# Optimization experiments

Hardware: AMD Instinct MI355X
Metric: run time of the kernel (lower is better)

Reference implementation:

```python
import jax, jax.numpy as jnp
import numpy as np

B, S, D = 2, 2048, 1024
H, HD = 16, 64          # num_heads, head_dim = D // H
C = 8                   # subspace_dim of the equivariant relative-position basis
EPS = 1e-6              # flax LayerNorm default epsilon


def setup_inputs() -> dict:
    key = jax.random.key(0)
    ks = jax.random.split(key, 12)
    sd = 0.02
    return {
        "x": jax.random.normal(ks[0], (B, S, D), jnp.float32),
        "Q_basis": jax.random.normal(ks[1], (S, S, C), jnp.float32),
        "Wq": jax.random.normal(ks[2], (D, H, HD), jnp.float32) * sd,
        "bq": jnp.zeros((H, HD), jnp.float32),
        "Wk": jax.random.normal(ks[3], (D, H, HD), jnp.float32) * sd,
        "bk": jnp.zeros((H, HD), jnp.float32),
        "Wv": jax.random.normal(ks[4], (D, H, HD), jnp.float32) * sd,
        "bv": jnp.zeros((H, HD), jnp.float32),
        "q_ln_scale": jnp.ones((HD,), jnp.float32),
        "k_ln_scale": jnp.ones((HD,), jnp.float32),
        "relative_attn": jax.random.normal(ks[5], (C, H), jnp.float32) * sd,
        "Wo": jax.random.normal(ks[6], (H, HD, D), jnp.float32) * sd,
        "bo": jnp.zeros((D,), jnp.float32),
    }


def _layernorm(x, scale):
    # LayerNorm over last axis, use_bias=False
    mu = jnp.mean(x, axis=-1, keepdims=True)
    var = jnp.mean(jnp.square(x - mu), axis=-1, keepdims=True)
    return (x - mu) * jax.lax.rsqrt(var + EPS) * scale


def reference(x, Q_basis, Wq, bq, Wk, bk, Wv, bv,
              q_ln_scale, k_ln_scale, relative_attn, Wo, bo):
    # QKV projections: [B,S,D] x [D,H,HD] -> [B,S,H,HD]
    q = jnp.einsum('bsd,dhk->bshk', x, Wq) + bq
    k = jnp.einsum('bsd,dhk->bshk', x, Wk) + bk
    v = jnp.einsum('bsd,dhk->bshk', x, Wv) + bv
    # QK layernorm over head_dim
    q = _layernorm(q, q_ln_scale)
    k = _layernorm(k, k_ln_scale)
    # Learned relative-position bias: [C,H] x [S,S,C] -> [H,S,S]
    bias = jnp.einsum('ch,qkc->hqk', relative_attn, Q_basis)
    # Scaled dot-product attention with bias (matches nn.dot_product_attention)
    scores = jnp.einsum('bqhd,bkhd->bhqk', q, k) / jnp.sqrt(jnp.float32(HD))
    attn = jax.nn.softmax(scores + bias, axis=-1)
    ctx = jnp.einsum('bhqk,bkhd->bqhd', attn, v)
    # Output projection over (heads, head_dim) -> D
    return jnp.einsum('bqhd,hdo->bqo', ctx, Wo) + bo
```

## Files before the change

kernel.cpp:

```cpp
#include <hip/hip_runtime.h>

typedef float f32x4 __attribute__((ext_vector_type(4)));
typedef __bf16 bf16x8 __attribute__((ext_vector_type(8)));
typedef unsigned short u16x8 __attribute__((ext_vector_type(8)));
typedef unsigned short u16x4 __attribute__((ext_vector_type(4)));

#define AS1 __attribute__((address_space(1)))
#define AS3 __attribute__((address_space(3)))

static __device__ __forceinline__ void gll16(const void* g, void* l) {
  __builtin_amdgcn_global_load_lds((const AS1 void*)g, (AS3 void*)l, 16, 0, 0);
}

static __device__ __forceinline__ float bf2f(unsigned short u) {
  unsigned int x = ((unsigned int)u) << 16;
  float f; __builtin_memcpy(&f, &x, 4); return f;
}
static __device__ __forceinline__ unsigned short f2bf(float f) {
  unsigned int x; __builtin_memcpy(&x, &f, 4);
  unsigned int r = (x + 0x7fffu + ((x >> 16) & 1u)) >> 16;
  return (unsigned short)r;
}

#define LOG2E 1.4426950408889634f
#define QSCALE (0.125f * LOG2E)

__global__ __launch_bounds__(256) void k_cvt_x(const float* __restrict__ x,
                                               unsigned short* __restrict__ xb) {
  int i = (blockIdx.x * 256 + threadIdx.x) * 4;
  float4 v = *(const float4*)(x + i);
  u16x4 o; o.x = f2bf(v.x); o.y = f2bf(v.y); o.z = f2bf(v.z); o.w = f2bf(v.w);
  *(u16x4*)(xb + i) = o;
}

__global__ __launch_bounds__(256) void k_transpose(const float* __restrict__ w0,
                                                   const float* __restrict__ w1,
                                                   const float* __restrict__ w2,
                                                   const float* __restrict__ w3,
                                                   unsigned short* __restrict__ dqkv,
                                                   unsigned short* __restrict__ dwo) {
  __shared__ float tile[32][33];
  int z = blockIdx.z;
  const float* src = (z == 0) ? w0 : (z == 1) ? w1 : (z == 2) ? w2 : w3;
  unsigned short* dst = (z < 3) ? (dqkv + (size_t)z * 1024 * 1024) : dwo;
  int tx = threadIdx.x, ty = threadIdx.y;
  int x0 = blockIdx.x * 32, y0 = blockIdx.y * 32;
#pragma unroll
  for (int i = 0; i < 4; ++i)
    tile[ty + 8 * i][tx] = src[(size_t)(y0 + ty + 8 * i) * 1024 + x0 + tx];
  __syncthreads();
#pragma unroll
  for (int i = 0; i < 4; ++i)
    dst[(size_t)(x0 + ty + 8 * i) * 1024 + y0 + tx] = f2bf(tile[tx][ty + 8 * i]);
}

__global__ __launch_bounds__(256) void k_bias(const float* __restrict__ Qb,
                                              const float* __restrict__ R,
                                              unsigned short* __restrict__ bias) {
  __shared__ float Rs[8][16];
  int t = threadIdx.x;
  if (t < 128) Rs[t >> 4][t & 15] = R[t] * LOG2E;
  __syncthreads();
  int q = blockIdx.x;
  int k = t * 8;
  const float* src = Qb + ((size_t)q * 2048 + k) * 8;
  float a[8][8];
#pragma unroll
  for (int kk = 0; kk < 8; ++kk) {
    float4 lo = *(const float4*)(src + kk * 8);
    float4 hi = *(const float4*)(src + kk * 8 + 4);
    a[kk][0] = lo.x; a[kk][1] = lo.y; a[kk][2] = lo.z; a[kk][3] = lo.w;
    a[kk][4] = hi.x; a[kk][5] = hi.y; a[kk][6] = hi.z; a[kk][7] = hi.w;
  }
#pragma unroll
  for (int h = 0; h < 16; ++h) {
    u16x8 o;
#pragma unroll
    for (int kk = 0; kk < 8; ++kk) {
      float s = 0.f;
#pragma unroll
      for (int c = 0; c < 8; ++c) s += a[kk][c] * Rs[c][h];
      o[kk] = f2bf(s);
    }
    *(u16x8*)(bias + ((size_t)h * 2048 + q) * 2048 + k) = o;
  }
}

__global__ __launch_bounds__(256) void k_qkv(const unsigned short* __restrict__ xb,
                                             const unsigned short* __restrict__ wt,
                                             const float* __restrict__ bq,
                                             const float* __restrict__ bk,
                                             const float* __restrict__ bv,
                                             const float* __restrict__ qls,
                                             const float* __restrict__ kls,
                                             unsigned short* __restrict__ qo,
                                             unsigned short* __restrict__ kqo,
                                             unsigned short* __restrict__ vo) {
  __shared__ unsigned short As[4096];
  __shared__ unsigned short Bs[4096];
  const int tid = threadIdx.x;
  const int w = tid >> 6, lane = tid & 63, quad = lane >> 4, lx = lane & 15;
  const int m0 = blockIdx.y * 128, n0 = blockIdx.x * 128;
  const int wrow = w >> 1, wcol = w & 1;

  f32x4 acc[4][4];
#pragma unroll
  for (int i = 0; i < 4; ++i)
#pragma unroll
    for (int j = 0; j < 4; ++j) acc[i][j] = (f32x4){0.f, 0.f, 0.f, 0.f};

  const unsigned short* ga = xb + (size_t)(m0 + 32 * w + (lane >> 2)) * 1024 + (lane & 3) * 8;
  const unsigned short* gb = wt + (size_t)(n0 + 32 * w + (lane >> 2)) * 1024 + (lane & 3) * 8;
  unsigned short* la = As + w * 1024;
  unsigned short* lb = Bs + w * 1024;

  for (int kt = 0; kt < 32; ++kt) {
    const int kofs = kt * 32;
    gll16(ga + kofs, la);
    gll16(ga + kofs + 16 * 1024, la + 512);
    gll16(gb + kofs, lb);
    gll16(gb + kofs + 16 * 1024, lb + 512);
    __syncthreads();
    bf16x8 af[4], bfr[4];
#pragma unroll
    for (int i = 0; i < 4; ++i)
      af[i] = *(const bf16x8*)&As[(64 * wrow + 16 * i + lx) * 32 + quad * 8];
#pragma unroll
    for (int j = 0; j < 4; ++j)
      bfr[j] = *(const bf16x8*)&Bs[(64 * wcol + 16 * j + lx) * 32 + quad * 8];
#pragma unroll
    for (int i = 0; i < 4; ++i)
#pragma unroll
      for (int j = 0; j < 4; ++j)
        acc[i][j] = __builtin_amdgcn_mfma_f32_16x16x32_bf16(af[i], bfr[j], acc[i][j], 0, 0, 0);
    __syncthreads();
  }

  const int colbase = n0 + 64 * wcol;
  const int region = colbase >> 10;
  const int h = (colbase & 1023) >> 6;
  const float* pbp = (region == 0) ? bq : (region == 1) ? bk : bv;
  float pb[4];
#pragma unroll
  for (int j = 0; j < 4; ++j) pb[j] = pbp[h * 64 + j * 16 + lx];

  if (region == 2) {
#pragma unroll
    for (int i = 0; i < 4; ++i) {
#pragma unroll
      for (int rr = 0; rr < 4; ++rr) {
        int m = m0 + 64 * wrow + 16 * i + quad * 4 + rr;
        int b = m >> 11, s = m & 2047;
        unsigned short* dst = vo + ((size_t)b * 16 + h) * 64 * 2048 + s;
#pragma unroll
        for (int j = 0; j < 4; ++j)
          dst[(size_t)(j * 16 + lx) * 2048] = f2bf(acc[i][j][rr] + pb[j]);
      }
    }
  } else {
    const float fac = region ? 1.0f : QSCALE;
    float scl[4];
    const float* lsp = region ? kls : qls;
#pragma unroll
    for (int j = 0; j < 4; ++j) scl[j] = lsp[j * 16 + lx] * fac;
    unsigned short* base = region ? kqo : qo;
#pragma unroll
    for (int i = 0; i < 4; ++i) {
#pragma unroll
      for (int rr = 0; rr < 4; ++rr) {
        int m = m0 + 64 * wrow + 16 * i + quad * 4 + rr;
        int b = m >> 11, s = m & 2047;
        float v0 = acc[i][0][rr] + pb[0];
        float v1 = acc[i][1][rr] + pb[1];
        float v2 = acc[i][2][rr] + pb[2];
        float v3 = acc[i][3][rr] + pb[3];
        float s1 = v0 + v1 + v2 + v3;
        float s2 = v0 * v0 + v1 * v1 + v2 * v2 + v3 * v3;
#pragma unroll
        for (int d = 1; d < 16; d <<= 1) {
          s1 += __shfl_xor(s1, d, 64);
          s2 += __shfl_xor(s2, d, 64);
        }
        float mu = s1 * 0.015625f;
        float var = s2 * 0.015625f - mu * mu;
        float ri = __builtin_amdgcn_rsqf(var + 1e-6f);
        unsigned short* dst = base + (((size_t)b * 16 + h) * 2048 + s) * 64;
        dst[0 * 16 + lx] = f2bf((v0 - mu) * ri * scl[0]);
        dst[1 * 16 + lx] = f2bf((v1 - mu) * ri * scl[1]);
        dst[2 * 16 + lx] = f2bf((v2 - mu) * ri * scl[2]);
        dst[3 * 16 + lx] = f2bf((v3 - mu) * ri * scl[3]);
      }
    }
  }
}

__global__ __launch_bounds__(256) void k_attn(const unsigned short* __restrict__ qp,
                                              const unsigned short* __restrict__ kp,
                                              const unsigned short* __restrict__ vp,
                                              const unsigned short* __restrict__ bp,
                                              unsigned short* __restrict__ ctx) {
  __shared__ unsigned short Qs[4096];
  __shared__ unsigned short Ks[4096];
  __shared__ unsigned short Vs[4096];
  __shared__ unsigned short Ps[4608];
  const int tid = threadIdx.x;
  const int w = tid >> 6, lane = tid & 63, quad = lane >> 4, lx = lane & 15;
  const int lx7 = lane & 7;
  const int qt = blockIdx.x, h = blockIdx.y, b = blockIdx.z;
  const int q0 = qt * 64;
  const size_t bh = (size_t)b * 16 + h;

  const unsigned short* qg = qp + (bh * 2048 + q0) * 64;
  gll16(qg + w * 512 + lane * 8, Qs + w * 512);
  gll16(qg + 2048 + w * 512 + lane * 8, Qs + 2048 + w * 512);
  __syncthreads();
  bf16x8 qf[2];
#pragma unroll
  for (int hh = 0; hh < 2; ++hh)
    qf[hh] = *(const bf16x8*)&Qs[(16 * w + lx) * 64 + hh * 32 + quad * 8];

  const unsigned short* kg = kp + bh * 2048 * 64;
  const unsigned short* vg = vp + bh * 64 * 2048;
  const unsigned short* bg = bp + ((size_t)h * 2048 + q0 + 16 * w + quad * 4) * 2048 + lx;

  const int rA = 16 * w + (lane >> 3);
  const int cA = (lane & 7) ^ (rA & 7);
  const unsigned short* kgA = kg + (size_t)rA * 64 + cA * 8;
  const unsigned short* kgB = kg + (size_t)(rA + 8) * 64 + cA * 8;
  const unsigned short* vgA = vg + (size_t)rA * 2048 + cA * 8;
  const unsigned short* vgB = vg + (size_t)(rA + 8) * 2048 + cA * 8;
  unsigned short* ldKA = Ks + w * 1024;
  unsigned short* ldKB = Ks + w * 1024 + 512;
  unsigned short* ldVA = Vs + w * 1024;
  unsigned short* ldVB = Vs + w * 1024 + 512;

  float l_run[4] = {0.f, 0.f, 0.f, 0.f};
  f32x4 acco[4];
#pragma unroll
  for (int j = 0; j < 4; ++j) acco[j] = (f32x4){0.f, 0.f, 0.f, 0.f};

  for (int kt = 0; kt < 32; ++kt) {
    const int k0 = kt * 64;
    gll16(kgA + (size_t)k0 * 64, ldKA);
    gll16(kgB + (size_t)k0 * 64, ldKB);
    gll16(vgA + k0, ldVA);
    gll16(vgB + k0, ldVB);
    unsigned short bu[4][4];
#pragma unroll
    for (int rr = 0; rr < 4; ++rr)
#pragma unroll
      for (int j = 0; j < 4; ++j) bu[rr][j] = bg[(size_t)rr * 2048 + k0 + j * 16];
    __syncthreads();

    f32x4 accs[4];
#pragma unroll
    for (int j = 0; j < 4; ++j)
#pragma unroll
      for (int rr = 0; rr < 4; ++rr) accs[j][rr] = bf2f(bu[rr][j]);
#pragma unroll
    for (int j = 0; j < 4; ++j) {
#pragma unroll
      for (int hh = 0; hh < 2; ++hh) {
        bf16x8 kf = *(const bf16x8*)&Ks[(j * 16 + lx) * 64 + ((hh * 4 + quad) ^ lx7) * 8];
        accs[j] = __builtin_amdgcn_mfma_f32_16x16x32_bf16(qf[hh], kf, accs[j], 0, 0, 0);
      }
    }
#pragma unroll
    for (int rr = 0; rr < 4; ++rr) {
      float p0 = __builtin_amdgcn_exp2f(accs[0][rr]);
      float p1 = __builtin_amdgcn_exp2f(accs[1][rr]);
      float p2 = __builtin_amdgcn_exp2f(accs[2][rr]);
      float p3 = __builtin_amdgcn_exp2f(accs[3][rr]);
      l_run[rr] += (p0 + p1) + (p2 + p3);
      unsigned short* pw = Ps + w * 1152 + (quad * 4 + rr) * 72 + lx;
      pw[0]  = f2bf(p0);
      pw[16] = f2bf(p1);
      pw[32] = f2bf(p2);
      pw[48] = f2bf(p3);
    }
    __asm__ volatile("s_waitcnt lgkmcnt(0)" ::: "memory");
    bf16x8 pf[2];
#pragma unroll
    for (int kh = 0; kh < 2; ++kh)
      pf[kh] = *(const bf16x8*)&Ps[w * 1152 + lx * 72 + kh * 32 + quad * 8];
#pragma unroll
    for (int j = 0; j < 4; ++j) {
#pragma unroll
      for (int kh = 0; kh < 2; ++kh) {
        bf16x8 vf = *(const bf16x8*)&Vs[(j * 16 + lx) * 64 + ((kh * 4 + quad) ^ lx7) * 8];
        acco[j] = __builtin_amdgcn_mfma_f32_16x16x32_bf16(pf[kh], vf, acco[j], 0, 0, 0);
      }
    }
    __syncthreads();
  }

#pragma unroll
  for (int rr = 0; rr < 4; ++rr) {
    float l = l_run[rr];
#pragma unroll
    for (int d = 1; d < 16; d <<= 1) l += __shfl_xor(l, d, 64);
    float rl = __builtin_amdgcn_rcpf(l);
    int s = q0 + 16 * w + quad * 4 + rr;
    unsigned short* dst = ctx + (((size_t)b * 2048 + s) * 16 + h) * 64;
#pragma unroll
    for (int j = 0; j < 4; ++j) dst[j * 16 + lx] = f2bf(acco[j][rr] * rl);
  }
}

__global__ __launch_bounds__(256) void k_out(const unsigned short* __restrict__ cx,
                                             const unsigned short* __restrict__ wt,
                                             const float* __restrict__ bo,
                                             float* __restrict__ out) {
  __shared__ unsigned short As[4096];
  __shared__ unsigned short Bs[4096];
  const int tid = threadIdx.x;
  const int w = tid >> 6, lane = tid & 63, quad = lane >> 4, lx = lane & 15;
  const int m0 = blockIdx.y * 128, n0 = blockIdx.x * 128;
  const int wrow = w >> 1, wcol = w & 1;

  f32x4 acc[4][4];
#pragma unroll
  for (int i = 0; i < 4; ++i)
#pragma unroll
    for (int j = 0; j < 4; ++j) acc[i][j] = (f32x4){0.f, 0.f, 0.f, 0.f};

  const unsigned short* ga = cx + (size_t)(m0 + 32 * w + (lane >> 2)) * 1024 + (lane & 3) * 8;
  const unsigned short* gb = wt + (size_t)(n0 + 32 * w + (lane >> 2)) * 1024 + (lane & 3) * 8;
  unsigned short* la = As + w * 1024;
  unsigned short* lb = Bs + w * 1024;

  for (int kt = 0; kt < 32; ++kt) {
    const int kofs = kt * 32;
    gll16(ga + kofs, la);
    gll16(ga + kofs + 16 * 1024, la + 512);
    gll16(gb + kofs, lb);
    gll16(gb + kofs + 16 * 1024, lb + 512);
    __syncthreads();
    bf16x8 af[4], bfr[4];
#pragma unroll
    for (int i = 0; i < 4; ++i)
      af[i] = *(const bf16x8*)&As[(64 * wrow + 16 * i + lx) * 32 + quad * 8];
#pragma unroll
    for (int j = 0; j < 4; ++j)
      bfr[j] = *(const bf16x8*)&Bs[(64 * wcol + 16 * j + lx) * 32 + quad * 8];
#pragma unroll
    for (int i = 0; i < 4; ++i)
#pragma unroll
      for (int j = 0; j < 4; ++j)
        acc[i][j] = __builtin_amdgcn_mfma_f32_16x16x32_bf16(af[i], bfr[j], acc[i][j], 0, 0, 0);
    __syncthreads();
  }

  const int colbase = n0 + 64 * wcol;
  float bb[4];
#pragma unroll
  for (int j = 0; j < 4; ++j) bb[j] = bo[colbase + j * 16 + lx];
#pragma unroll
  for (int i = 0; i < 4; ++i) {
#pragma unroll
    for (int rr = 0; rr < 4; ++rr) {
      int m = m0 + 64 * wrow + 16 * i + quad * 4 + rr;
      float* dst = out + (size_t)m * 1024 + colbase;
#pragma unroll
      for (int j = 0; j < 4; ++j) dst[j * 16 + lx] = acc[i][j][rr] + bb[j];
    }
  }
}

extern "C" void kernel_launch(void* const* d_in, const int* in_sizes, int n_in,
                              void* d_out, int out_size, void* d_ws, size_t ws_size,
                              hipStream_t stream) {
  (void)in_sizes; (void)n_in; (void)out_size; (void)ws_size;
  const float* x   = (const float*)d_in[0];
  const float* Qb  = (const float*)d_in[1];
  const float* Wq  = (const float*)d_in[2];
  const float* bq  = (const float*)d_in[3];
  const float* Wk  = (const float*)d_in[4];
  const float* bk  = (const float*)d_in[5];
  const float* Wv  = (const float*)d_in[6];
  const float* bv  = (const float*)d_in[7];
  const float* qls = (const float*)d_in[8];
  const float* kls = (const float*)d_in[9];
  const float* Ra  = (const float*)d_in[10];
  const float* Wo  = (const float*)d_in[11];
  const float* bo  = (const float*)d_in[12];
  float* out = (float*)d_out;

  char* ws = (char*)d_ws;
  unsigned short* xb    = (unsigned short*)(ws + 0);
  unsigned short* wqkvt = (unsigned short*)(ws + 8388608);
  unsigned short* wot   = (unsigned short*)(ws + 14680064);
  unsigned short* qb    = (unsigned short*)(ws + 16777216);
  unsigned short* kb    = (unsigned short*)(ws + 25165824);
  unsigned short* vtb   = (unsigned short*)(ws + 33554432);
  unsigned short* ctxb  = (unsigned short*)(ws + 41943040);
  unsigned short* biasb = (unsigned short*)(ws + 50331648);

  k_cvt_x<<<4096, 256, 0, stream>>>(x, xb);
  k_transpose<<<dim3(32, 32, 4), dim3(32, 8), 0, stream>>>(Wq, Wk, Wv, Wo, wqkvt, wot);
  k_bias<<<2048, 256, 0, stream>>>(Qb, Ra, biasb);
  k_qkv<<<dim3(24, 32), 256, 0, stream>>>(xb, wqkvt, bq, bk, bv, qls, kls, qb, kb, vtb);
  k_attn<<<dim3(32, 16, 2), 256, 0, stream>>>(qb, kb, vtb, biasb, ctxb);
  k_out<<<dim3(8, 32), 256, 0, stream>>>(ctxb, wot, bo, out);
}
```

Baseline: 454.4 us.

## Double-buffer LDS tiles in QKV, attention and output kernels with prefetch

Converts the GEMM and attention K/V loops to double-buffered LDS, issuing the global-to-LDS loads for the next tile before computing on the current one. The bias values for the next tile are also prefetched into registers. Q and P now share one LDS buffer, which keeps the extra LDS within budget, and P gets an XOR swizzle instead of padding. s_setprio is raised around the MFMA blocks. The aim is to hide global memory latency, at the cost of more LDS and registers, which may lower occupancy.

After: 436.0 us. 1.04x faster.

```diff
diff --git a/kernel.cpp b/kernel.cpp
--- a/kernel.cpp
+++ b/kernel.cpp
@@ -96,8 +96,8 @@
                                              unsigned short* __restrict__ qo,
                                              unsigned short* __restrict__ kqo,
                                              unsigned short* __restrict__ vo) {
-  __shared__ unsigned short As[4096];
-  __shared__ unsigned short Bs[4096];
+  __shared__ __align__(16) unsigned short As[8192];
+  __shared__ __align__(16) unsigned short Bs[8192];
   const int tid = threadIdx.x;
   const int w = tid >> 6, lane = tid & 63, quad = lane >> 4, lx = lane & 15;
   const int m0 = blockIdx.y * 128, n0 = blockIdx.x * 128;
@@ -111,28 +111,40 @@
 
   const unsigned short* ga = xb + (size_t)(m0 + 32 * w + (lane >> 2)) * 1024 + (lane & 3) * 8;
   const unsigned short* gb = wt + (size_t)(n0 + 32 * w + (lane >> 2)) * 1024 + (lane & 3) * 8;
-  unsigned short* la = As + w * 1024;
-  unsigned short* lb = Bs + w * 1024;
+
+  gll16(ga, As + w * 1024);
+  gll16(ga + 16 * 1024, As + w * 1024 + 512);
+  gll16(gb, Bs + w * 1024);
+  gll16(gb + 16 * 1024, Bs + w * 1024 + 512);
+  __syncthreads();
 
   for (int kt = 0; kt < 32; ++kt) {
-    const int kofs = kt * 32;
-    gll16(ga + kofs, la);
-    gll16(ga + kofs + 16 * 1024, la + 512);
-    gll16(gb + kofs, lb);
-    gll16(gb + kofs + 16 * 1024, lb + 512);
-    __syncthreads();
+    const int cur = kt & 1;
+    if (kt < 31) {
+      const int kofs = (kt + 1) * 32;
+      unsigned short* lan = As + (cur ^ 1) * 4096 + w * 1024;
+      unsigned short* lbn = Bs + (cur ^ 1) * 4096 + w * 1024;
+      gll16(ga + kofs, lan);
+      gll16(ga + kofs + 16 * 1024, lan + 512);
+      gll16(gb + kofs, lbn);
+      gll16(gb + kofs + 16 * 1024, lbn + 512);
+    }
+    const unsigned short* ac = As + cur * 4096;
+    const unsigned short* bc = Bs + cur * 4096;
     bf16x8 af[4], bfr[4];
 #pragma unroll
     for (int i = 0; i < 4; ++i)
-      af[i] = *(const bf16x8*)&As[(64 * wrow + 16 * i + lx) * 32 + quad * 8];
+      af[i] = *(const bf16x8*)&ac[(64 * wrow + 16 * i + lx) * 32 + quad * 8];
 #pragma unroll
     for (int j = 0; j < 4; ++j)
-      bfr[j] = *(const bf16x8*)&Bs[(64 * wcol + 16 * j + lx) * 32 + quad * 8];
+      bfr[j] = *(const bf16x8*)&bc[(64 * wcol + 16 * j + lx) * 32 + quad * 8];
+    __builtin_amdgcn_s_setprio(1);
 #pragma unroll
     for (int i = 0; i < 4; ++i)
 #pragma unroll
       for (int j = 0; j < 4; ++j)
         acc[i][j] = __builtin_amdgcn_mfma_f32_16x16x32_bf16(af[i], bfr[j], acc[i][j], 0, 0, 0);
+    __builtin_amdgcn_s_setprio(0);
     __syncthreads();
   }
 
@@ -199,10 +211,9 @@
                                               const unsigned short* __restrict__ vp,
                                               const unsigned short* __restrict__ bp,
                                               unsigned short* __restrict__ ctx) {
-  __shared__ unsigned short Qs[4096];
-  __shared__ unsigned short Ks[4096];
-  __shared__ unsigned short Vs[4096];
-  __shared__ unsigned short Ps[4608];
+  __shared__ __align__(16) unsigned short QPs[4096];
+  __shared__ __align__(16) unsigned short Ks[8192];
+  __shared__ __align__(16) unsigned short Vs[8192];
   const int tid = threadIdx.x;
   const int w = tid >> 6, lane = tid & 63, quad = lane >> 4, lx = lane & 15;
   const int lx7 = lane & 7;
@@ -211,13 +222,8 @@
   const size_t bh = (size_t)b * 16 + h;
 
   const unsigned short* qg = qp + (bh * 2048 + q0) * 64;
-  gll16(qg + w * 512 + lane * 8, Qs + w * 512);
-  gll16(qg + 2048 + w * 512 + lane * 8, Qs + 2048 + w * 512);
-  __syncthreads();
-  bf16x8 qf[2];
-#pragma unroll
-  for (int hh = 0; hh < 2; ++hh)
-    qf[hh] = *(const bf16x8*)&Qs[(16 * w + lx) * 64 + hh * 32 + quad * 8];
+  gll16(qg + w * 512 + lane * 8, QPs + w * 512);
+  gll16(qg + 2048 + w * 512 + lane * 8, QPs + 2048 + w * 512);
 
   const unsigned short* kg = kp + bh * 2048 * 64;
   const unsigned short* vg = vp + bh * 64 * 2048;
@@ -229,10 +235,23 @@
   const unsigned short* kgB = kg + (size_t)(rA + 8) * 64 + cA * 8;
   const unsigned short* vgA = vg + (size_t)rA * 2048 + cA * 8;
   const unsigned short* vgB = vg + (size_t)(rA + 8) * 2048 + cA * 8;
-  unsigned short* ldKA = Ks + w * 1024;
-  unsigned short* ldKB = Ks + w * 1024 + 512;
-  unsigned short* ldVA = Vs + w * 1024;
-  unsigned short* ldVB = Vs + w * 1024 + 512;
+
+  gll16(kgA, Ks + w * 1024);
+  gll16(kgB, Ks + w * 1024 + 512);
+  gll16(vgA, Vs + w * 1024);
+  gll16(vgB, Vs + w * 1024 + 512);
+  unsigned short bu[4][4], bun[4][4];
+#pragma unroll
+  for (int rr = 0; rr < 4; ++rr)
+#pragma unroll
+    for (int j = 0; j < 4; ++j) bu[rr][j] = bg[(size_t)rr * 2048 + j * 16];
+
+  __syncthreads();
+
+  bf16x8 qf[2];
+#pragma unroll
+  for (int hh = 0; hh < 2; ++hh)
+    qf[hh] = *(const bf16x8*)&QPs[(16 * w + lx) * 64 + hh * 32 + quad * 8];
 
   float l_run[4] = {0.f, 0.f, 0.f, 0.f};
   f32x4 acco[4];
@@ -240,31 +259,39 @@
   for (int j = 0; j < 4; ++j) acco[j] = (f32x4){0.f, 0.f, 0.f, 0.f};
 
   for (int kt = 0; kt < 32; ++kt) {
-    const int k0 = kt * 64;
-    gll16(kgA + (size_t)k0 * 64, ldKA);
-    gll16(kgB + (size_t)k0 * 64, ldKB);
-    gll16(vgA + k0, ldVA);
-    gll16(vgB + k0, ldVB);
-    unsigned short bu[4][4];
-#pragma unroll
-    for (int rr = 0; rr < 4; ++rr)
-#pragma unroll
-      for (int j = 0; j < 4; ++j) bu[rr][j] = bg[(size_t)rr * 2048 + k0 + j * 16];
-    __syncthreads();
+    const int cur = kt & 1;
+    const unsigned short* kc = Ks + cur * 4096;
+    const unsigned short* vc = Vs + cur * 4096;
+    if (kt < 31) {
+      const size_t k1 = (size_t)(kt + 1) * 64;
+      unsigned short* kn = Ks + (cur ^ 1) * 4096 + w * 1024;
+      unsigned short* vn = Vs + (cur ^ 1) * 4096 + w * 1024;
+      gll16(kgA + k1 * 64, kn);
+      gll16(kgB + k1 * 64, kn + 512);
+      gll16(vgA + k1, vn);
+      gll16(vgB + k1, vn + 512);
+#pragma unroll
+      for (int rr = 0; rr < 4; ++rr)
+#pragma unroll
+        for (int j = 0; j < 4; ++j) bun[rr][j] = bg[(size_t)rr * 2048 + k1 + j * 16];
+    }
 
     f32x4 accs[4];
 #pragma unroll
     for (int j = 0; j < 4; ++j)
 #pragma unroll
       for (int rr = 0; rr < 4; ++rr) accs[j][rr] = bf2f(bu[rr][j]);
+    __builtin_amdgcn_s_setprio(1);
 #pragma unroll
     for (int j = 0; j < 4; ++j) {
 #pragma unroll
       for (int hh = 0; hh < 2; ++hh) {
-        bf16x8 kf = *(const bf16x8*)&Ks[(j * 16 + lx) * 64 + ((hh * 4 + quad) ^ lx7) * 8];
+        bf16x8 kf = *(const bf16x8*)&kc[(j * 16 + lx) * 64 + ((hh * 4 + quad) ^ lx7) * 8];
         accs[j] = __builtin_amdgcn_mfma_f32_16x16x32_bf16(qf[hh], kf, accs[j], 0, 0, 0);
       }
     }
+    __builtin_amdgcn_s_setprio(0);
+
 #pragma unroll
     for (int rr = 0; rr < 4; ++rr) {
       float p0 = __builtin_amdgcn_exp2f(accs[0][rr]);
@@ -272,26 +299,35 @@
       float p2 = __builtin_amdgcn_exp2f(accs[2][rr]);
       float p3 = __builtin_amdgcn_exp2f(accs[3][rr]);
       l_run[rr] += (p0 + p1) + (p2 + p3);
-      unsigned short* pw = Ps + w * 1152 + (quad * 4 + rr) * 72 + lx;
-      pw[0]  = f2bf(p0);
-      pw[16] = f2bf(p1);
-      pw[32] = f2bf(p2);
-      pw[48] = f2bf(p3);
+      const int q = quad * 4 + rr;
+      const int swz = q & 7;
+      const int ch = lx >> 3;
+      unsigned short* pw = QPs + w * 1024 + q * 64 + (lx & 7);
+      pw[((ch ^ swz) << 3)]       = f2bf(p0);
+      pw[(((ch + 2) ^ swz) << 3)] = f2bf(p1);
+      pw[(((ch + 4) ^ swz) << 3)] = f2bf(p2);
+      pw[(((ch + 6) ^ swz) << 3)] = f2bf(p3);
     }
     __asm__ volatile("s_waitcnt lgkmcnt(0)" ::: "memory");
     bf16x8 pf[2];
 #pragma unroll
     for (int kh = 0; kh < 2; ++kh)
-      pf[kh] = *(const bf16x8*)&Ps[w * 1152 + lx * 72 + kh * 32 + quad * 8];
+      pf[kh] = *(const bf16x8*)&QPs[w * 1024 + lx * 64 + (((kh * 4 + quad) ^ (lx & 7)) << 3)];
+    __builtin_amdgcn_s_setprio(1);
 #pragma unroll
     for (int j = 0; j < 4; ++j) {
 #pragma unroll
       for (int kh = 0; kh < 2; ++kh) {
-        bf16x8 vf = *(const bf16x8*)&Vs[(j * 16 + lx) * 64 + ((kh * 4 + quad) ^ lx7) * 8];
+        bf16x8 vf = *(const bf16x8*)&vc[(j * 16 + lx) * 64 + ((kh * 4 + quad) ^ lx7) * 8];
         acco[j] = __builtin_amdgcn_mfma_f32_16x16x32_bf16(pf[kh], vf, acco[j], 0, 0, 0);
       }
     }
+    __builtin_amdgcn_s_setprio(0);
     __syncthreads();
+#pragma unroll
+    for (int rr = 0; rr < 4; ++rr)
+#pragma unroll
+      for (int j = 0; j < 4; ++j) bu[rr][j] = bun[rr][j];
   }
 
 #pragma unroll
@@ -311,8 +347,8 @@
                                              const unsigned short* __restrict__ wt,
                                              const float* __restrict__ bo,
                                              float* __restrict__ out) {
-  __shared__ unsigned short As[4096];
-  __shared__ unsigned short Bs[4096];
+  __shared__ __align__(16) unsigned short As[8192];
+  __shared__ __align__(16) unsigned short Bs[8192];
   const int tid = threadIdx.x;
   const int w = tid >> 6, lane = tid & 63, quad = lane >> 4, lx = lane & 15;
   const int m0 = blockIdx.y * 128, n0 = blockIdx.x * 128;
@@ -326,28 +362,40 @@
 
   const unsigned short* ga = cx + (size_t)(m0 + 32 * w + (lane >> 2)) * 1024 + (lane & 3) * 8;
   const unsigned short* gb = wt + (size_t)(n0 + 32 * w + (lane >> 2)) * 1024 + (lane & 3) * 8;
-  unsigned short* la = As + w * 1024;
-  unsigned short* lb = Bs + w * 1024;
+
+  gll16(ga, As + w * 1024);
+  gll16(ga + 16 * 1024, As + w * 1024 + 512);
+  gll16(gb, Bs + w * 1024);
+  gll16(gb + 16 * 1024, Bs + w * 1024 + 512);
+  __syncthreads();
 
   for (int kt = 0; kt < 32; ++kt) {
-    const int kofs = kt * 32;
-    gll16(ga + kofs, la);
-    gll16(ga + kofs + 16 * 1024, la + 512);
-    gll16(gb + kofs, lb);
-    gll16(gb + kofs + 16 * 1024, lb + 512);
-    __syncthreads();
+    const int cur = kt & 1;
+    if (kt < 31) {
+      const int kofs = (kt + 1) * 32;
+      unsigned short* lan = As + (cur ^ 1) * 4096 + w * 1024;
+      unsigned short* lbn = Bs + (cur ^ 1) * 4096 + w * 1024;
+      gll16(ga + kofs, lan);
+      gll16(ga + kofs + 16 * 1024, lan + 512);
+      gll16(gb + kofs, lbn);
+      gll16(gb + kofs + 16 * 1024, lbn + 512);
+    }
+    const unsigned short* ac = As + cur * 4096;
+    const unsigned short* bc = Bs + cur * 4096;
     bf16x8 af[4], bfr[4];
 #pragma unroll
     for (int i = 0; i < 4; ++i)
-      af[i] = *(const bf16x8*)&As[(64 * wrow + 16 * i + lx) * 32 + quad * 8];
+      af[i] = *(const bf16x8*)&ac[(64 * wrow + 16 * i + lx) * 32 + quad * 8];
 #pragma unroll
     for (int j = 0; j < 4; ++j)
-      bfr[j] = *(const bf16x8*)&Bs[(64 * wcol + 16 * j + lx) * 32 + quad * 8];
+      bfr[j] = *(const bf16x8*)&bc[(64 * wcol + 16 * j + lx) * 32 + quad * 8];
+    __builtin_amdgcn_s_setprio(1);
 #pragma unroll
     for (int i = 0; i < 4; ++i)
 #pragma unroll
       for (int j = 0; j < 4; ++j)
         acc[i][j] = __builtin_amdgcn_mfma_f32_16x16x32_bf16(af[i], bfr[j], acc[i][j], 0, 0, 0);
+    __builtin_amdgcn_s_setprio(0);
     __syncthreads();
   }
 
```
